# Kernel tuning notes

Hardware: AMD Instinct MI355X
Metric: run time of the kernel (lower is better)

The kernel has to match this reference:

```python
import jax, jax.numpy as jnp
import numpy as np

DIM = 256
HEADS = 8
DIM_FF = 1024
N = 4096
HEAD_DIM = DIM // HEADS
SCALE = HEAD_DIM ** -0.5


def layer_norm(x, gamma, beta, eps=1e-5):
    mu = jnp.mean(x, axis=-1, keepdims=True)
    var = jnp.var(x, axis=-1, keepdims=True)
    return (x - mu) * jax.lax.rsqrt(var + eps) * gamma + beta


def setup_inputs() -> dict:
    key = jax.random.key(0)
    ks = jax.random.split(key, 8)
    x = jax.random.normal(ks[0], (N, DIM), dtype=jnp.float32)
    adj = jax.random.randint(ks[1], (N, N), 0, 2, dtype=jnp.int32)
    adj = adj.at[jnp.arange(N), jnp.arange(N)].set(1)  # self-loops
    s = 1.0 / np.sqrt(DIM)
    w_qkv = jax.random.normal(ks[2], (DIM, 3 * DIM), dtype=jnp.float32) * s
    w_proj = jax.random.normal(ks[3], (DIM, DIM), dtype=jnp.float32) * s
    b_proj = jnp.zeros((DIM,), jnp.float32)
    w1 = jax.random.normal(ks[4], (DIM, DIM_FF), dtype=jnp.float32) * s
    b1 = jnp.zeros((DIM_FF,), jnp.float32)
    w2 = jax.random.normal(ks[5], (DIM_FF, DIM), dtype=jnp.float32) / np.sqrt(DIM_FF)
    b2 = jnp.zeros((DIM,), jnp.float32)
    g1 = jnp.ones((DIM,), jnp.float32)
    be1 = jnp.zeros((DIM,), jnp.float32)
    g2 = jnp.ones((DIM,), jnp.float32)
    be2 = jnp.zeros((DIM,), jnp.float32)
    return {"x": x, "adj": adj, "w_qkv": w_qkv, "w_proj": w_proj,
            "b_proj": b_proj, "w1": w1, "b1": b1, "w2": w2, "b2": b2,
            "g1": g1, "be1": be1, "g2": g2, "be2": be2}


def reference(x, adj, w_qkv, w_proj, b_proj, w1, b1, w2, b2, g1, be1, g2, be2):
    n = x.shape[0]
    qkv = layer_norm(x, g1, be1) @ w_qkv            # (N, 3*dim)
    qkv = qkv.reshape(n, 3, HEADS, HEAD_DIM)
    q, k, v = qkv[:, 0], qkv[:, 1], qkv[:, 2]       # (N, h, d)
    scores = jnp.einsum('nhd,mhd->hnm', q, k) * SCALE
    mask = (adj != 0)[None, :, :]                    # (1, N, N)
    scores = jnp.where(mask, scores, -jnp.inf)
    attn = jax.nn.softmax(scores, axis=-1)           # (h, N, N)
    out = jnp.einsum('hnm,mhd->nhd', attn, v).reshape(n, DIM)
    x = x + out @ w_proj + b_proj
    h2 = layer_norm(x, g2, be2)
    ff = jax.nn.gelu(h2 @ w1 + b1) @ w2 + b2
    return x + ff
```

## Files before the change

### kernel.cpp

```cpp
#include <hip/hip_runtime.h>
#include <hip/hip_bf16.h>

#define NT 4096
#define DM 256
#define NH 8
#define HD 32
#define DFF 1024

typedef __attribute__((ext_vector_type(8))) short s8v;
typedef __attribute__((ext_vector_type(4))) float f4v;
typedef __attribute__((ext_vector_type(2))) float f2v;
typedef __attribute__((ext_vector_type(16))) float f16v;
typedef __attribute__((ext_vector_type(4))) int i4v;

static __device__ __forceinline__ unsigned short f2b(float f){
  union{float f; unsigned u;} v; v.f=f;
  return (unsigned short)((v.u + 0x7FFFu + ((v.u>>16)&1u))>>16);
}

__global__ __launch_bounds__(256) void prologue_kernel(
    const int* __restrict__ adj, unsigned long long* __restrict__ mask,
    const float* __restrict__ wqkv, const float* __restrict__ wproj,
    const float* __restrict__ w1, const float* __restrict__ w2,
    unsigned short* __restrict__ wqkvT, unsigned short* __restrict__ wprojT,
    unsigned short* __restrict__ w1T, unsigned short* __restrict__ w2T,
    const float* __restrict__ x, const float* __restrict__ g1,
    const float* __restrict__ be1, unsigned short* __restrict__ h1){
  int bx = blockIdx.x;
  if (bx < 1024){
    int wv = threadIdx.x>>6, lane = threadIdx.x&63;
    int base = (bx*4 + wv)*64;
    for (int it=0; it<16; ++it){
      int w0 = base + it*4;
      unsigned long long b0 = __ballot(adj[(long)(w0+0)*64 + lane]!=0);
      unsigned long long b1 = __ballot(adj[(long)(w0+1)*64 + lane]!=0);
      unsigned long long b2 = __ballot(adj[(long)(w0+2)*64 + lane]!=0);
      unsigned long long b3 = __ballot(adj[(long)(w0+3)*64 + lane]!=0);
      if (lane==0){ mask[w0]=b0; mask[w0+1]=b1; mask[w0+2]=b2; mask[w0+3]=b3; }
    }
  } else if (bx < 1152){
    int t = (bx-1024)*256 + threadIdx.x;
    const int stride = 128*256;
    for (int i=t;i<768*DM;i+=stride){int n=i>>8,k=i&255; wqkvT[i]=f2b(wqkv[k*768+n]);}
    for (int i=t;i<DM*DM;i+=stride){int n=i>>8,k=i&255; wprojT[i]=f2b(wproj[k*DM+n]);}
    for (int i=t;i<DFF*DM;i+=stride){int n=i>>8,k=i&255; w1T[i]=f2b(w1[k*DFF+n]);}
    for (int i=t;i<DM*DFF;i+=stride){int n=i/DFF,k=i-n*DFF; w2T[i]=f2b(w2[k*DM+n]);}
  } else {
    int wv = threadIdx.x>>6, lane = threadIdx.x&63;
    int rbase = (bx-1152)*4 + wv;
    for (int j=0;j<8;j++){
      int row = rbase + j*512;
      float4 v = *(const float4*)(x + row*DM + lane*4);
      float s = v.x+v.y+v.z+v.w;
      float sq = v.x*v.x+v.y*v.y+v.z*v.z+v.w*v.w;
      #pragma unroll
      for (int m=1;m<64;m<<=1){ s += __shfl_xor(s,m); sq += __shfl_xor(sq,m); }
      float mu = s*(1.0f/DM);
      float rs = rsqrtf(sq*(1.0f/DM) - mu*mu + 1e-5f);
      float4 gv = *(const float4*)(g1 + lane*4);
      float4 bv = *(const float4*)(be1 + lane*4);
      ushort4 o;
      o.x = f2b((v.x-mu)*rs*gv.x + bv.x);
      o.y = f2b((v.y-mu)*rs*gv.y + bv.y);
      o.z = f2b((v.z-mu)*rs*gv.z + bv.z);
      o.w = f2b((v.w-mu)*rs*gv.w + bv.w);
      *(ushort4*)(h1 + row*DM + lane*4) = o;
    }
  }
}

template<int KD, int MODE>
__global__ __launch_bounds__(256,4) void gemm24(const unsigned short* __restrict__ A,
            const unsigned short* __restrict__ Wt, const float* __restrict__ bias,
            void* __restrict__ outp,
            unsigned short* __restrict__ Qp, unsigned short* __restrict__ Kp,
            unsigned short* __restrict__ Vt){
  int wv = threadIdx.x>>6, lane = threadIdx.x&63;
  int lo = lane&15, hi = lane>>4;
  int r0 = blockIdx.y*32;
  int cbase = blockIdx.x*256 + wv*16;
  const unsigned short* ar0 = A + (r0+lo)*KD + hi*8;
  const unsigned short* ar1 = ar0 + 16*KD;
  const unsigned short* br0 = Wt + (cbase     +lo)*KD + hi*8;
  const unsigned short* br1 = Wt + (cbase+ 64 +lo)*KD + hi*8;
  const unsigned short* br2 = Wt + (cbase+128 +lo)*KD + hi*8;
  const unsigned short* br3 = Wt + (cbase+192 +lo)*KD + hi*8;
  f4v c00={0,0,0,0},c01={0,0,0,0},c02={0,0,0,0},c03={0,0,0,0};
  f4v c10={0,0,0,0},c11={0,0,0,0},c12={0,0,0,0},c13={0,0,0,0};
  #pragma unroll 2
  for (int k0=0;k0<KD;k0+=32){
    s8v a0 = *(const s8v*)(ar0 + k0);
    s8v a1 = *(const s8v*)(ar1 + k0);
    s8v b0 = *(const s8v*)(br0 + k0);
    s8v b1 = *(const s8v*)(br1 + k0);
    s8v b2 = *(const s8v*)(br2 + k0);
    s8v b3 = *(const s8v*)(br3 + k0);
    c00 = __builtin_amdgcn_mfma_f32_16x16x32_bf16(a0,b0,c00,0,0,0);
    c10 = __builtin_amdgcn_mfma_f32_16x16x32_bf16(a1,b0,c10,0,0,0);
    c01 = __builtin_amdgcn_mfma_f32_16x16x32_bf16(a0,b1,c01,0,0,0);
    c11 = __builtin_amdgcn_mfma_f32_16x16x32_bf16(a1,b1,c11,0,0,0);
    c02 = __builtin_amdgcn_mfma_f32_16x16x32_bf16(a0,b2,c02,0,0,0);
    c12 = __builtin_amdgcn_mfma_f32_16x16x32_bf16(a1,b2,c12,0,0,0);
    c03 = __builtin_amdgcn_mfma_f32_16x16x32_bf16(a0,b3,c03,0,0,0);
    c13 = __builtin_amdgcn_mfma_f32_16x16x32_bf16(a1,b3,c13,0,0,0);
  }
  const float scl2 = (float)(0.17677669529663687 * 1.4426950408889634);
  #pragma unroll
  for (int rt=0;rt<2;rt++){
    f4v e0 = rt? c10:c00, e1 = rt? c11:c01, e2 = rt? c12:c02, e3 = rt? c13:c03;
    int nb = r0 + rt*16 + hi*4;
    #pragma unroll
    for (int jj=0;jj<4;jj++){
      f4v acc = jj==0?e0 : jj==1?e1 : jj==2?e2 : e3;
      int c = cbase + jj*64 + lo;
      if (MODE==0){
        int which = c>>8, hd = c&255, hh = hd>>5, d = hd&31;
        #pragma unroll
        for (int r=0;r<4;r++){
          int n = nb + r;
          float val = acc[r];
          if (which==0) Qp[(hh*NT+n)*HD+d]=f2b(val*scl2);
          else if (which==1) Kp[(hh*NT+n)*HD+d]=f2b(val);
          else Vt[(hh*HD+d)*NT+n]=f2b(val);
        }
      }
    }
  }
}

__global__ __launch_bounds__(512,2) void attn_kernel(
    const unsigned short* __restrict__ Q, const unsigned short* __restrict__ K,
    const unsigned short* __restrict__ Vt, const unsigned* __restrict__ mb32,
    unsigned short* __restrict__ out){
  __shared__ float Opart[8][32][34];
  __shared__ float llS[8][32];
  int wv = threadIdx.x>>6, lane = threadIdx.x&63;
  int l31 = lane&31, hi5 = lane>>5;
  int h = blockIdx.x, q0 = blockIdx.y*64;
  const unsigned short* QbA = Q + (h*NT + q0 + l31)*HD + hi5*8;
  const unsigned short* QbB = QbA + 32*HD;
  s8v bqA1 = *(const s8v*)(QbA);
  s8v bqA2 = *(const s8v*)(QbA + 16);
  s8v bqB1 = *(const s8v*)(QbB);
  s8v bqB2 = *(const s8v*)(QbB + 16);
  const unsigned short* Kb = K + h*NT*HD;
  const unsigned short* Vb = Vt + (h*HD + l31)*NT;
  const unsigned* mrowA = mb32 + (q0+l31)*(NT/32) + wv*16;
  const unsigned* mrowB = mrowA + 32*(NT/32);
  const float C0 = -11.541560327111707f;
  const f16v c0v = {C0,C0,C0,C0,C0,C0,C0,C0,C0,C0,C0,C0,C0,C0,C0,C0};
  f2v lacA = {0.f,0.f}, lacB = {0.f,0.f};
  f16v accA = {0,0,0,0,0,0,0,0,0,0,0,0,0,0,0,0};
  f16v accB = {0,0,0,0,0,0,0,0,0,0,0,0,0,0,0,0};
  union SU { f16v v; f2v p[8]; };
  const unsigned short* Kt0 = Kb + (wv*512 + l31)*HD + hi5*8;
  s8v kc1 = *(const s8v*)(Kt0);
  s8v kc2 = *(const s8v*)(Kt0 + 16);
  for (int tg=0; tg<4; tg++){
    i4v mw4A = *(const i4v*)(mrowA + tg*4);
    i4v mw4B = *(const i4v*)(mrowB + tg*4);
    #pragma unroll
    for (int ti=0; ti<4; ti++){
      int t = tg*4 + ti;
      int m0 = wv*512 + t*32;
      const unsigned short* Vtp = Vb + m0 + hi5*8;
      s8v av1 = *(const s8v*)(Vtp);
      s8v av2 = *(const s8v*)(Vtp + 16);
      int tn = (t<15)? t+1 : 15;
      const unsigned short* Ktn = Kb + (wv*512 + tn*32 + l31)*HD + hi5*8;
      s8v kn1 = *(const s8v*)(Ktn);
      s8v kn2 = *(const s8v*)(Ktn + 16);
      SU sa, sb;
      __builtin_amdgcn_s_setprio(1);
      sa.v = __builtin_amdgcn_mfma_f32_32x32x16_bf16(kc1, bqA1, c0v, 0,0,0);
      sa.v = __builtin_amdgcn_mfma_f32_32x32x16_bf16(kc2, bqA2, sa.v, 0,0,0);
      sb.v = __builtin_amdgcn_mfma_f32_32x32x16_bf16(kc1, bqB1, c0v, 0,0,0);
      sb.v = __builtin_amdgcn_mfma_f32_32x32x16_bf16(kc2, bqB2, sb.v, 0,0,0);
      __builtin_amdgcn_s_setprio(0);
      unsigned mwA = ((unsigned)mw4A[ti]) >> (4*hi5);
      unsigned mwB = ((unsigned)mw4B[ti]) >> (4*hi5);
      #pragma unroll
      for (int r=0;r<16;r++){
        int bp = (r&3)+8*(r>>2);
        float pa = __builtin_amdgcn_exp2f(sa.v[r]);
        float pb = __builtin_amdgcn_exp2f(sb.v[r]);
        sa.v[r] = ((mwA >> bp) & 1u) ? pa : 0.0f;
        sb.v[r] = ((mwB >> bp) & 1u) ? pb : 0.0f;
      }
      #pragma unroll
      for (int i=0;i<8;i++){ lacA += sa.p[i]; lacB += sb.p[i]; }
      unsigned a0,a1,a2,a3,a4,a5,a6,a7, b0,b1,b2,b3,b4,b5,b6,b7;
      asm("v_cvt_pk_bf16_f32 %0, %1, %2" : "=v"(a0) : "v"(sa.v[0]),  "v"(sa.v[1]));
      asm("v_cvt_pk_bf16_f32 %0, %1, %2" : "=v"(a1) : "v"(sa.v[2]),  "v"(sa.v[3]));
      asm("v_cvt_pk_bf16_f32 %0, %1, %2" : "=v"(a2) : "v"(sa.v[4]),  "v"(sa.v[5]));
      asm("v_cvt_pk_bf16_f32 %0, %1, %2" : "=v"(a3) : "v"(sa.v[6]),  "v"(sa.v[7]));
      asm("v_cvt_pk_bf16_f32 %0, %1, %2" : "=v"(a4) : "v"(sa.v[8]),  "v"(sa.v[9]));
      asm("v_cvt_pk_bf16_f32 %0, %1, %2" : "=v"(a5) : "v"(sa.v[10]), "v"(sa.v[11]));
      asm("v_cvt_pk_bf16_f32 %0, %1, %2" : "=v"(a6) : "v"(sa.v[12]), "v"(sa.v[13]));
      asm("v_cvt_pk_bf16_f32 %0, %1, %2" : "=v"(a7) : "v"(sa.v[14]), "v"(sa.v[15]));
      asm("v_permlane32_swap_b32 %0, %1" : "+v"(a0), "+v"(a2));
      asm("v_permlane32_swap_b32 %0, %1" : "+v"(a1), "+v"(a3));
      asm("v_permlane32_swap_b32 %0, %1" : "+v"(a4), "+v"(a6));
      asm("v_permlane32_swap_b32 %0, %1" : "+v"(a5), "+v"(a7));
      asm("v_cvt_pk_bf16_f32 %0, %1, %2" : "=v"(b0) : "v"(sb.v[0]),  "v"(sb.v[1]));
      asm("v_cvt_pk_bf16_f32 %0, %1, %2" : "=v"(b1) : "v"(sb.v[2]),  "v"(sb.v[3]));
      asm("v_cvt_pk_bf16_f32 %0, %1, %2" : "=v"(b2) : "v"(sb.v[4]),  "v"(sb.v[5]));
      asm("v_cvt_pk_bf16_f32 %0, %1, %2" : "=v"(b3) : "v"(sb.v[6]),  "v"(sb.v[7]));
      asm("v_cvt_pk_bf16_f32 %0, %1, %2" : "=v"(b4) : "v"(sb.v[8]),  "v"(sb.v[9]));
      asm("v_cvt_pk_bf16_f32 %0, %1, %2" : "=v"(b5) : "v"(sb.v[10]), "v"(sb.v[11]));
      asm("v_cvt_pk_bf16_f32 %0, %1, %2" : "=v"(b6) : "v"(sb.v[12]), "v"(sb.v[13]));
      asm("v_cvt_pk_bf16_f32 %0, %1, %2" : "=v"(b7) : "v"(sb.v[14]), "v"(sb.v[15]));
      asm("v_permlane32_swap_b32 %0, %1" : "+v"(b0), "+v"(b2));
      asm("v_permlane32_swap_b32 %0, %1" : "+v"(b1), "+v"(b3));
      asm("v_permlane32_swap_b32 %0, %1" : "+v"(b4), "+v"(b6));
      asm("v_permlane32_swap_b32 %0, %1" : "+v"(b5), "+v"(b7));
      i4v pA1i = {(int)a0,(int)a1,(int)a2,(int)a3};
      i4v pA2i = {(int)a4,(int)a5,(int)a6,(int)a7};
      i4v pB1i = {(int)b0,(int)b1,(int)b2,(int)b3};
      i4v pB2i = {(int)b4,(int)b5,(int)b6,(int)b7};
      s8v pA1 = __builtin_bit_cast(s8v, pA1i);
      s8v pA2 = __builtin_bit_cast(s8v, pA2i);
      s8v pB1 = __builtin_bit_cast(s8v, pB1i);
      s8v pB2 = __builtin_bit_cast(s8v, pB2i);
      __builtin_amdgcn_s_setprio(1);
      accA = __builtin_amdgcn_mfma_f32_32x32x16_bf16(av1, pA1, accA, 0,0,0);
      accA = __builtin_amdgcn_mfma_f32_32x32x16_bf16(av2, pA2, accA, 0,0,0);
      accB = __builtin_amdgcn_mfma_f32_32x32x16_bf16(av1, pB1, accB, 0,0,0);
      accB = __builtin_amdgcn_mfma_f32_32x32x16_bf16(av2, pB2, accB, 0,0,0);
      __builtin_amdgcn_s_setprio(0);
      kc1 = kn1; kc2 = kn2;
    }
  }
  int tid = threadIdx.x;
  int qq = tid>>4, dd = 2*(tid&15);
  #pragma unroll
  for (int i=0;i<8;i++){
    int d = (2*i&3) + 8*(i>>1) + 4*hi5;
    float2 p2; p2.x = accA[2*i]; p2.y = accA[2*i+1];
    *(float2*)&Opart[wv][l31][d] = p2;
  }
  float lsumA = lacA[0] + lacA[1];
  lsumA += __shfl_xor(lsumA, 32);
  if (hi5==0) llS[wv][l31] = lsumA;
  __syncthreads();
  {
    float L=0.f, o0=0.f, o1=0.f;
    #pragma unroll
    for (int u=0;u<8;u++){
      L  += llS[u][qq];
      o0 += Opart[u][qq][dd];
      o1 += Opart[u][qq][dd+1];
    }
    float inv = 1.0f/L;
    float r0 = o0*inv, r1 = o1*inv;
    unsigned pw;
    asm("v_cvt_pk_bf16_f32 %0, %1, %2" : "=v"(pw) : "v"(r0), "v"(r1));
    *(unsigned*)(out + (q0+qq)*DM + h*HD + dd) = pw;
  }
  __syncthreads();
  #pragma unroll
  for (int i=0;i<8;i++){
    int d = (2*i&3) + 8*(i>>1) + 4*hi5;
    float2 p2; p2.x = accB[2*i]; p2.y = accB[2*i+1];
    *(float2*)&Opart[wv][l31][d] = p2;
  }
  float lsumB = lacB[0] + lacB[1];
  lsumB += __shfl_xor(lsumB, 32);
  if (hi5==0) llS[wv][l31] = lsumB;
  __syncthreads();
  {
    float L=0.f, o0=0.f, o1=0.f;
    #pragma unroll
    for (int u=0;u<8;u++){
      L  += llS[u][qq];
      o0 += Opart[u][qq][dd];
      o1 += Opart[u][qq][dd+1];
    }
    float inv = 1.0f/L;
    float r0 = o0*inv, r1 = o1*inv;
    unsigned pw;
    asm("v_cvt_pk_bf16_f32 %0, %1, %2" : "=v"(pw) : "v"(r0), "v"(r1));
    *(unsigned*)(out + (q0+32+qq)*DM + h*HD + dd) = pw;
  }
}

__global__ __launch_bounds__(512,2) void tail_kernel(
    const unsigned short* __restrict__ ao, const unsigned short* __restrict__ wprojT,
    const float* __restrict__ bproj, const float* __restrict__ x,
    const float* __restrict__ g2, const float* __restrict__ be2,
    const unsigned short* __restrict__ w1T, const float* __restrict__ b1,
    const unsigned short* __restrict__ w2T, const float* __restrict__ b2,
    float* __restrict__ outp){
  __shared__ unsigned short h2L[16][DM];
  __shared__ unsigned short gL[16][DFF];
  __shared__ float Ss[8][16], Sq[8][16];
  int wv = threadIdx.x>>6, lane = threadIdx.x&63;
  int lo = lane&15, hi = lane>>4;
  int r0 = blockIdx.x*16;
  float t[2][4];

  {
    const unsigned short* ar  = ao + (r0+lo)*DM + hi*8;
    const unsigned short* pb0 = wprojT + (wv*16     +lo)*DM + hi*8;
    const unsigned short* pb1 = wprojT + (wv*16+128 +lo)*DM + hi*8;
    f4v a0={0,0,0,0}, a1={0,0,0,0};
    #pragma unroll
    for (int k0=0;k0<DM;k0+=32){
      s8v a = *(const s8v*)(ar + k0);
      a0 = __builtin_amdgcn_mfma_f32_16x16x32_bf16(a, *(const s8v*)(pb0+k0), a0,0,0,0);
      a1 = __builtin_amdgcn_mfma_f32_16x16x32_bf16(a, *(const s8v*)(pb1+k0), a1,0,0,0);
    }
    float sr[4]={0,0,0,0}, sq[4]={0,0,0,0};
    #pragma unroll
    for (int jj=0;jj<2;jj++){
      f4v acc = jj? a1 : a0;
      int c = jj*128 + wv*16 + lo;
      float bc = bproj[c];
      #pragma unroll
      for (int r=0;r<4;r++){
        int n = r0 + hi*4 + r;
        float tv = acc[r] + bc + x[n*DM+c];
        t[jj][r] = tv; sr[r] += tv; sq[r] += tv*tv;
      }
    }
    #pragma unroll
    for (int m=1;m<16;m<<=1){
      #pragma unroll
      for (int r=0;r<4;r++){ sr[r]+=__shfl_xor(sr[r],m); sq[r]+=__shfl_xor(sq[r],m); }
    }
    if (lo==0){
      #pragma unroll
      for (int r=0;r<4;r++){ Ss[wv][hi*4+r]=sr[r]; Sq[wv][hi*4+r]=sq[r]; }
    }
    __syncthreads();
    #pragma unroll
    for (int r=0;r<4;r++){
      int nl = hi*4+r;
      float S=0.f, Qs=0.f;
      #pragma unroll
      for (int u=0;u<8;u++){ S += Ss[u][nl]; Qs += Sq[u][nl]; }
      float mu = S*(1.0f/DM);
      float rs = rsqrtf(Qs*(1.0f/DM) - mu*mu + 1e-5f);
      #pragma unroll
      for (int jj=0;jj<2;jj++){
        int c = jj*128 + wv*16 + lo;
        unsigned short hv = f2b((t[jj][r]-mu)*rs*g2[c] + be2[c]);
        int g = c>>3;
        h2L[nl][((g^(nl&7))<<3) + (c&7)] = hv;
      }
    }
  }
  __syncthreads();

  #pragma unroll
  for (int p=0;p<2;p++){
    int cb = p*512 + wv*16;
    const unsigned short* wb0 = w1T + (cb      +lo)*DM + hi*8;
    const unsigned short* wb1 = w1T + (cb+128  +lo)*DM + hi*8;
    const unsigned short* wb2 = w1T + (cb+256  +lo)*DM + hi*8;
    const unsigned short* wb3 = w1T + (cb+384  +lo)*DM + hi*8;
    f4v c0={0,0,0,0},c1={0,0,0,0},c2={0,0,0,0},c3={0,0,0,0};
    #pragma unroll
    for (int k0=0;k0<DM;k0+=32){
      s8v a = *(const s8v*)&h2L[lo][(((hi + (k0>>3)) ^ (lo&7))<<3)];
      c0 = __builtin_amdgcn_mfma_f32_16x16x32_bf16(a, *(const s8v*)(wb0+k0), c0,0,0,0);
      c1 = __builtin_amdgcn_mfma_f32_16x16x32_bf16(a, *(const s8v*)(wb1+k0), c1,0,0,0);
      c2 = __builtin_amdgcn_mfma_f32_16x16x32_bf16(a, *(const s8v*)(wb2+k0), c2,0,0,0);
      c3 = __builtin_amdgcn_mfma_f32_16x16x32_bf16(a, *(const s8v*)(wb3+k0), c3,0,0,0);
    }
    #pragma unroll
    for (int jj=0;jj<4;jj++){
      f4v acc = jj==0?c0 : jj==1?c1 : jj==2?c2 : c3;
      int c = p*512 + jj*128 + wv*16 + lo;
      float bc = b1[c];
      #pragma unroll
      for (int r=0;r<4;r++){
        int nl = hi*4+r;
        float xx = acc[r] + bc;
        float x2v = xx*xx;
        float arg = xx*(2.302340531f + 0.102952640f*x2v);
        float e  = __builtin_amdgcn_exp2f(arg);
        float rcp = __builtin_amdgcn_rcpf(e + 1.0f);
        unsigned short gv = f2b(xx - xx*rcp);
        int g = c>>3;
        gL[nl][((g^(nl&7))<<3) + (c&7)] = gv;
      }
    }
  }
  __syncthreads();

  {
    const unsigned short* db0 = w2T + (wv*16     +lo)*DFF + hi*8;
    const unsigned short* db1 = w2T + (wv*16+128 +lo)*DFF + hi*8;
    f4v e0={0,0,0,0}, e1={0,0,0,0};
    #pragma unroll 4
    for (int k0=0;k0<DFF;k0+=32){
      s8v a = *(const s8v*)&gL[lo][(((hi + (k0>>3)) ^ (lo&7))<<3)];
      e0 = __builtin_amdgcn_mfma_f32_16x16x32_bf16(a, *(const s8v*)(db0+k0), e0,0,0,0);
      e1 = __builtin_amdgcn_mfma_f32_16x16x32_bf16(a, *(const s8v*)(db1+k0), e1,0,0,0);
    }
    #pragma unroll
    for (int jj=0;jj<2;jj++){
      f4v acc = jj? e1 : e0;
      int c = jj*128 + wv*16 + lo;
      float bc = b2[c];
      #pragma unroll
      for (int r=0;r<4;r++){
        int n = r0 + hi*4 + r;
        outp[n*DM+c] = acc[r] + bc + t[jj][r];
      }
    }
  }
}

extern "C" void kernel_launch(void* const* d_in, const int* in_sizes, int n_in,
                              void* d_out, int out_size, void* d_ws, size_t ws_size,
                              hipStream_t stream){
  const float* x     = (const float*)d_in[0];
  const int*   adj   = (const int*)d_in[1];
  const float* wqkv  = (const float*)d_in[2];
  const float* wproj = (const float*)d_in[3];
  const float* bproj = (const float*)d_in[4];
  const float* w1    = (const float*)d_in[5];
  const float* b1    = (const float*)d_in[6];
  const float* w2    = (const float*)d_in[7];
  const float* b2    = (const float*)d_in[8];
  const float* g1    = (const float*)d_in[9];
  const float* be1   = (const float*)d_in[10];
  const float* g2    = (const float*)d_in[11];
  const float* be2   = (const float*)d_in[12];

  char* ws = (char*)d_ws;
  unsigned short* h1    = (unsigned short*)(ws + (0u<<20));
  unsigned short* Qb    = (unsigned short*)(ws + (2u<<20));
  unsigned short* Kb    = (unsigned short*)(ws + (4u<<20));
  unsigned short* Vt    = (unsigned short*)(ws + (6u<<20));
  unsigned short* ao    = (unsigned short*)(ws + (8u<<20));
  unsigned short* wqkvT = (unsigned short*)(ws + (24u<<20));
  unsigned short* wprojT= (unsigned short*)(ws + (25u<<20));
  unsigned short* w1T   = (unsigned short*)(ws + (26u<<20));
  unsigned short* w2T   = (unsigned short*)(ws + (27u<<20));
  unsigned long long* mbits = (unsigned long long*)(ws + (28u<<20));
  float* outF = (float*)d_out;

  hipLaunchKernelGGL(prologue_kernel, dim3(1280), dim3(256), 0, stream,
                     adj, mbits, wqkv, wproj, w1, w2, wqkvT, wprojT, w1T, w2T,
                     x, g1, be1, h1);
  hipLaunchKernelGGL((gemm24<256,0>), dim3(3,128), dim3(256), 0, stream,
                     h1, wqkvT, nullptr, nullptr, Qb, Kb, Vt);
  hipLaunchKernelGGL(attn_kernel, dim3(8,64), dim3(512), 0, stream,
                     Qb, Kb, Vt, (const unsigned*)mbits, ao);
  hipLaunchKernelGGL(tail_kernel, dim3(256), dim3(512), 0, stream,
                     ao, wprojT, bproj, x, g2, be2, w1T, b1, w2T, b2, outF);
}
```

Measured before the change: 117.5 us.

## Double-buffer W2 tiles into LDS via global_load_lds in FFN second GEMM

```diff
diff --git a/kernel.cpp b/kernel.cpp
--- a/kernel.cpp
+++ b/kernel.cpp
@@ -16,6 +16,12 @@
 static __device__ __forceinline__ unsigned short f2b(float f){
   union{float f; unsigned u;} v; v.f=f;
   return (unsigned short)((v.u + 0x7FFFu + ((v.u>>16)&1u))>>16);
+}
+
+static __device__ __forceinline__ void gl_lds16(const void* g, void* l){
+  __builtin_amdgcn_global_load_lds(
+      (const __attribute__((address_space(1))) unsigned int*)g,
+      (__attribute__((address_space(3))) unsigned int*)l, 16, 0, 0);
 }
 
 __global__ __launch_bounds__(256) void prologue_kernel(
@@ -294,10 +300,21 @@
   __shared__ unsigned short h2L[16][DM];
   __shared__ unsigned short gL[16][DFF];
   __shared__ float Ss[8][16], Sq[8][16];
+  __shared__ __align__(16) unsigned char w2S[2][32768];
   int wv = threadIdx.x>>6, lane = threadIdx.x&63;
   int lo = lane&15, hi = lane>>4;
+  int tid = threadIdx.x;
   int r0 = blockIdx.x*16;
   float t[2][4];
+
+#define STAGE_W2(KT, BUF)                                                     \
+  { _Pragma("unroll")                                                         \
+    for (int rr=0; rr<4; ++rr){                                               \
+      int col_ = rr*64 + (tid>>3);                                            \
+      int ko_  = (tid&7) ^ (col_&7);                                          \
+      gl_lds16(w2T + col_*DFF + (KT)*64 + ko_*8,                              \
+               &w2S[BUF][rr*8192 + tid*16]);                                  \
+    } }
 
   {
     const unsigned short* ar  = ao + (r0+lo)*DM + hi*8;
@@ -351,6 +368,9 @@
     }
   }
   __syncthreads();
+
+  STAGE_W2(0, 0);
+  STAGE_W2(1, 1);
 
   #pragma unroll
   for (int p=0;p<2;p++){
@@ -390,14 +410,22 @@
   __syncthreads();
 
   {
-    const unsigned short* db0 = w2T + (wv*16     +lo)*DFF + hi*8;
-    const unsigned short* db1 = w2T + (wv*16+128 +lo)*DFF + hi*8;
     f4v e0={0,0,0,0}, e1={0,0,0,0};
-    #pragma unroll 4
-    for (int k0=0;k0<DFF;k0+=32){
-      s8v a = *(const s8v*)&gL[lo][(((hi + (k0>>3)) ^ (lo&7))<<3)];
-      e0 = __builtin_amdgcn_mfma_f32_16x16x32_bf16(a, *(const s8v*)(db0+k0), e0,0,0,0);
-      e1 = __builtin_amdgcn_mfma_f32_16x16x32_bf16(a, *(const s8v*)(db1+k0), e1,0,0,0);
+    int c0i = wv*16 + lo;
+    int c1i = c0i + 128;
+    for (int kt=0; kt<16; ++kt){
+      if (kt>=1 && kt<15) STAGE_W2(kt+1, (kt+1)&1);
+      const unsigned char* bufp = w2S[kt&1];
+      #pragma unroll
+      for (int ks=0; ks<2; ++ks){
+        int k0 = kt*64 + ks*32;
+        s8v a = *(const s8v*)&gL[lo][(((hi + (k0>>3)) ^ (lo&7))<<3)];
+        s8v b0 = *(const s8v*)(bufp + c0i*128 + ((((ks*4)+hi) ^ (c0i&7))<<4));
+        s8v b1 = *(const s8v*)(bufp + c1i*128 + ((((ks*4)+hi) ^ (c1i&7))<<4));
+        e0 = __builtin_amdgcn_mfma_f32_16x16x32_bf16(a, b0, e0,0,0,0);
+        e1 = __builtin_amdgcn_mfma_f32_16x16x32_bf16(a, b1, e1,0,0,0);
+      }
+      __syncthreads();
     }
     #pragma unroll
     for (int jj=0;jj<2;jj++){
@@ -411,6 +439,7 @@
       }
     }
   }
+#undef STAGE_W2
 }
 
 extern "C" void kernel_launch(void* const* d_in, const int* in_sizes, int n_in,
```

Result: faster. 113.3 us (-3.6%).
